# Kernel optimization log

Measured on AMD Instinct MI355X. Metric: run time of the kernel, lower is better.

## Reference

```python
import jax, jax.numpy as jnp
from jax import lax
import numpy as np

B, E, K, CAP = 512, 16, 2, 64
H = W = 32
ALPHA, LOAD_PEN, MIN_USE, RTEMP = 0.7, 2.0, 0.05, 1.0


def _conv(x, w, b):
    y = lax.conv_general_dilated(x, w, (1, 1), 'SAME', dimension_numbers=('NCHW', 'OIHW', 'NCHW'))
    return y + b[None, :, None, None]


def _bn(x, s, b):
    # eval-mode BatchNorm2d: running_mean=0, running_var=1 folded into scale/bias
    return x * s[None, :, None, None] + b[None, :, None, None]


def _ln(x, g, b, eps=1e-5):
    m = x.mean(-1, keepdims=True)
    v = ((x - m) ** 2).mean(-1, keepdims=True)
    return (x - m) * lax.rsqrt(v + eps) * g + b


def _maxpool(x):
    return lax.reduce_window(x, -jnp.inf, lax.max, (1, 1, 2, 2), (1, 1, 2, 2), 'VALID')


def setup_inputs() -> dict:
    key = jax.random.key(0)
    ks = iter(jax.random.split(key, 64))

    def nrm(shape, fan_in):
        return jax.random.normal(next(ks), shape, jnp.float32) / float(np.sqrt(fan_in))

    inp = {'x': jax.random.normal(next(ks), (B, 3, H, W), jnp.float32)}
    for i, (ci, co) in enumerate([(3, 64), (64, 64), (64, 128), (128, 128), (128, 256), (256, 256)], 1):
        inp[f'conv_w{i}'] = nrm((co, ci, 3, 3), ci * 9)
        inp[f'conv_b{i}'] = jnp.zeros((co,), jnp.float32)
        inp[f'bn_s{i}'] = jnp.ones((co,), jnp.float32)
        inp[f'bn_b{i}'] = jnp.zeros((co,), jnp.float32)
    inp['gate_w1'] = nrm((E, 64, 256), 256); inp['gate_b1'] = jnp.zeros((E, 64)); inp['gate_g1'] = jnp.ones((E, 64)); inp['gate_bb1'] = jnp.zeros((E, 64))
    inp['gate_w2'] = nrm((E, 32, 64), 64); inp['gate_b2'] = jnp.zeros((E, 32))
    inp['gate_w3'] = nrm((E, 1, 32), 32); inp['gate_b3'] = jnp.zeros((E, 1))
    inp['exp_w1'] = nrm((E, 256, 256), 256); inp['exp_b1'] = jnp.zeros((E, 256)); inp['exp_g1'] = jnp.ones((E, 256)); inp['exp_bb1'] = jnp.zeros((E, 256))
    inp['exp_w2'] = nrm((E, 128, 256), 256); inp['exp_b2'] = jnp.zeros((E, 128)); inp['exp_g2'] = jnp.ones((E, 128)); inp['exp_bb2'] = jnp.zeros((E, 128))
    inp['exp_w3'] = nrm((E, 128, 128), 128); inp['exp_b3'] = jnp.zeros((E, 128))
    inp['cls_w'] = nrm((E, 10, 128), 128); inp['cls_b'] = jnp.zeros((E, 10))
    return inp


def _forward(x, conv_w1, conv_b1, bn_s1, bn_b1, conv_w2, conv_b2, bn_s2, bn_b2,
             conv_w3, conv_b3, bn_s3, bn_b3, conv_w4, conv_b4, bn_s4, bn_b4,
             conv_w5, conv_b5, bn_s5, bn_b5, conv_w6, conv_b6, bn_s6, bn_b6,
             gate_w1, gate_b1, gate_g1, gate_bb1, gate_w2, gate_b2, gate_w3, gate_b3,
             exp_w1, exp_b1, exp_g1, exp_bb1, exp_w2, exp_b2, exp_g2, exp_bb2,
             exp_w3, exp_b3, cls_w, cls_b):
    # ---- trunk (eval: dropout = identity) ----
    h = jax.nn.relu(_bn(_conv(x, conv_w1, conv_b1), bn_s1, bn_b1))
    h = jax.nn.relu(_bn(_conv(h, conv_w2, conv_b2), bn_s2, bn_b2))
    h = _maxpool(h)
    h = jax.nn.relu(_bn(_conv(h, conv_w3, conv_b3), bn_s3, bn_b3))
    h = jax.nn.relu(_bn(_conv(h, conv_w4, conv_b4), bn_s4, bn_b4))
    h = _maxpool(h)
    h = jax.nn.relu(_bn(_conv(h, conv_w5, conv_b5), bn_s5, bn_b5))
    h = jax.nn.relu(_bn(_conv(h, conv_w6, conv_b6), bn_s6, bn_b6))
    feats = h.mean((2, 3))  # AdaptiveAvgPool2d(1) + Flatten -> [B, 256]
    # ---- experts (vectorized over E) ----
    h1 = jax.nn.relu(_ln(jnp.einsum('bc,eoc->beo', feats, exp_w1) + exp_b1, exp_g1, exp_bb1))
    h2 = jax.nn.relu(_ln(jnp.einsum('beh,eoh->beo', h1, exp_w2) + exp_b2, exp_g2, exp_bb2))
    embeds = jnp.einsum('beh,eoh->beo', h2, exp_w3) + exp_b3  # [B, E, 128]
    logits_e = jnp.einsum('bed,ecd->bec', embeds, cls_w) + cls_b  # [B, E, 10]
    probs = jax.nn.softmax(logits_e, axis=2)
    entropy = -(probs * jnp.log(probs + 1e-12)).sum(-1)  # [B, E]
    confidence = -entropy
    # ---- gates (vectorized over E) ----
    g1 = jax.nn.relu(_ln(jnp.einsum('bc,eoc->beo', feats, gate_w1) + gate_b1, gate_g1, gate_bb1))
    g2 = jax.nn.relu(jnp.einsum('beh,eoh->beo', g1, gate_w2) + gate_b2)
    scores = (jnp.einsum('beh,eoh->beo', g2, gate_w3) + gate_b3)[..., 0] / RTEMP  # [B, E]
    # ---- top-k capacity routing (eval: usage_ema at init = 1/E, no noise) ----
    usage = jnp.full((E,), 1.0 / E, jnp.float32)
    combined = ALPHA * scores + (1.0 - ALPHA) * confidence
    combined = combined + jnp.where(usage < MIN_USE, (MIN_USE - usage) * 10.0, 0.0)[None, :]
    balanced = combined - LOAD_PEN * usage[None, :]
    _, topk_idx = lax.top_k(balanced, K)  # [B, K]

    def step(loads, idx_row):
        lt = loads[idx_row]  # [K]
        avail = lt < CAP
        chosen = jnp.where(jnp.any(avail), idx_row[jnp.argmax(avail)], idx_row[jnp.argmin(lt)])
        return loads.at[chosen].add(1.0), chosen

    _, chosen = lax.scan(step, jnp.zeros((E,), jnp.float32), topk_idx)
    D = jax.nn.one_hot(chosen, E, dtype=jnp.bool_)  # [B, E]
    masked = jnp.where(D, balanced, -jnp.inf)
    rw = jax.nn.softmax(masked, axis=1) * D
    rw = rw / (rw.sum(1, keepdims=True) + 1e-12)
    final_logits = jnp.einsum('be,bec->bc', rw, logits_e)
    return final_logits, balanced, D


def reference(x, conv_w1, conv_b1, bn_s1, bn_b1, conv_w2, conv_b2, bn_s2, bn_b2,
              conv_w3, conv_b3, bn_s3, bn_b3, conv_w4, conv_b4, bn_s4, bn_b4,
              conv_w5, conv_b5, bn_s5, bn_b5, conv_w6, conv_b6, bn_s6, bn_b6,
              gate_w1, gate_b1, gate_g1, gate_bb1, gate_w2, gate_b2, gate_w3, gate_b3,
              exp_w1, exp_b1, exp_g1, exp_bb1, exp_w2, exp_b2, exp_g2, exp_bb2,
              exp_w3, exp_b3, cls_w, cls_b):
    return _forward(x, conv_w1, conv_b1, bn_s1, bn_b1, conv_w2, conv_b2, bn_s2, bn_b2,
                    conv_w3, conv_b3, bn_s3, bn_b3, conv_w4, conv_b4, bn_s4, bn_b4,
                    conv_w5, conv_b5, bn_s5, bn_b5, conv_w6, conv_b6, bn_s6, bn_b6,
                    gate_w1, gate_b1, gate_g1, gate_bb1, gate_w2, gate_b2, gate_w3, gate_b3,
                    exp_w1, exp_b1, exp_g1, exp_bb1, exp_w2, exp_b2, exp_g2, exp_bb2,
                    exp_w3, exp_b3, cls_w, cls_b)
```

## Files before the change

kernel.cpp:

```cpp
#include <hip/hip_runtime.h>


typedef _Float16 h16;
typedef _Float16 half8 __attribute__((ext_vector_type(8)));
typedef float f32x16 __attribute__((ext_vector_type(16)));

__device__ __forceinline__ void split2f(float x, h16& hh, h16& ll) {
  h16 a = (h16)x;
  hh = a;
  ll = (h16)(x - (float)a);
}

__global__ void prep_all_k(const float* __restrict__ cw1, const float* __restrict__ cw2,
                           const float* __restrict__ cw3, const float* __restrict__ cw4,
                           const float* __restrict__ cw5, const float* __restrict__ cw6,
                           float* __restrict__ wt1t, h16* __restrict__ wh,
                           h16* p0, h16* p1, h16* p2, h16* p3) {
  int idx = blockIdx.x * 256 + threadIdx.x;
  if (idx < 64) {
    h16* p = (idx < 16) ? p0 : (idx < 32) ? p1 : (idx < 48) ? p2 : p3;
    p[idx & 15] = (h16)0.f;
    return;
  }
  idx -= 64;
  if (idx < 1728) {
    int co = idx % 64, r = idx / 64;
    wt1t[idx] = cw1[(size_t)co * 27 + r];
    return;
  }
  idx -= 1728;
  const float* w; int CIN, COUT; size_t off;
  if (idx < 36864)        { w = cw2; CIN = 64;  COUT = 64;  off = 0; }
  else if (idx < 110592)  { w = cw3; CIN = 64;  COUT = 128; off = 36864;  idx -= 36864; }
  else if (idx < 258048)  { w = cw4; CIN = 128; COUT = 128; off = 110592; idx -= 110592; }
  else if (idx < 552960)  { w = cw5; CIN = 128; COUT = 256; off = 258048; idx -= 258048; }
  else if (idx < 1142784) { w = cw6; CIN = 256; COUT = 256; off = 552960; idx -= 552960; }
  else return;
  int KCOB = COUT >> 6;
  int lidx = idx;
  int c8   = idx & 7;
  int t    = idx >> 3;
  int co64 = t & 63;  t >>= 6;
  int half = t & 1;   t >>= 1;
  int cob  = t % KCOB; t /= KCOB;
  int tap  = t % 9;
  int ck   = t / 9;
  int ci = ck * 16 + half * 8 + c8;
  int co = cob * 64 + co64;
  float v = w[((size_t)co * CIN + ci) * 9 + tap];
  wh[off + lidx] = (h16)v;
}

__global__ __launch_bounds__(256) void conv1_k(
    const float* __restrict__ x, const float* __restrict__ wt,
    const float* __restrict__ cb, const float* __restrict__ bns,
    const float* __restrict__ bnb, h16* __restrict__ oh, h16* __restrict__ ol)
{
  __shared__ float sx[3 * 34 * 34];
  const int tid = threadIdx.x;
  const int img = blockIdx.x;
  for (int idx = tid; idx < 3 * 34 * 34; idx += 256) {
    int xx = idx % 34;
    int t  = idx / 34;
    int rr = t % 34;
    int c  = t / 34;
    int gr = rr - 1, gx = xx - 1;
    float v = 0.f;
    if (gr >= 0 && gr < 32 && gx >= 0 && gx < 32)
      v = x[((size_t)(img * 3 + c) * 32 + gr) * 32 + gx];
    sx[(c * 34 + rr) * 34 + xx] = v;
  }
  __syncthreads();
#pragma unroll 1
  for (int k = 0; k < 4; ++k) {
    int px = k * 256 + tid;
    int yy = px >> 5, xx = px & 31;
    float in27[27];
#pragma unroll
    for (int c = 0; c < 3; ++c)
#pragma unroll
      for (int dy = 0; dy < 3; ++dy)
#pragma unroll
        for (int dx = 0; dx < 3; ++dx)
          in27[c * 9 + dy * 3 + dx] = sx[(c * 34 + yy + dy) * 34 + xx + dx];
#pragma unroll 1
    for (int cbk = 0; cbk < 4; ++cbk) {
      h16 hb[16], lb[16];
#pragma unroll
      for (int j = 0; j < 16; ++j) {
        int co = cbk * 16 + j;
        float acc = 0.f;
#pragma unroll
        for (int t = 0; t < 27; ++t) acc = fmaf(in27[t], wt[t * 64 + co], acc);
        float s = bns[co];
        float yv = fmaxf(fmaf(acc + cb[co], s, bnb[co]), 0.f);
        split2f(yv, hb[j], lb[j]);
      }
      size_t o = 16 + ((size_t)(img * 4 + cbk) * 1024 + px) * 16;
      *(half8*)&oh[o]     = *(half8*)&hb[0];
      *(half8*)&oh[o + 8] = *(half8*)&hb[8];
      *(half8*)&ol[o]     = *(half8*)&lb[0];
      *(half8*)&ol[o + 8] = *(half8*)&lb[8];
    }
  }
}

template<int H, int W, int CIN, int COUT, int MT, int POOL, int OCC>
__global__ __launch_bounds__(256, OCC) void conv_mfma(
    const h16* __restrict__ Ah, const h16* __restrict__ Al,
    const h16* __restrict__ Wh,
    const float* __restrict__ cb, const float* __restrict__ bns,
    const float* __restrict__ bnb,
    h16* __restrict__ Oh, h16* __restrict__ Ol, float* __restrict__ feats)
{
  constexpr int TPI  = (H * W) / 32;
  constexpr int RPT  = 32 / W;
  constexpr int IPB  = (4 * MT * 32 >= H * W) ? (4 * MT * 32) / (H * W) : 1;
  constexpr int KC   = CIN / 16;
  constexpr int HW   = H * W;
  constexpr int KCO  = COUT / 16;
  constexpr int KCOB = COUT / 64;
  constexpr int LOGW = (W == 32) ? 5 : (W == 16) ? 4 : 3;
  constexpr int PF   = (MT == 1) ? 3 : 2;

  __shared__ h16 sBh[2][9 * 2 * 64 * 8];
  __shared__ float sRed[(POOL == 2 && MT == 1) ? 256 : 1];

  const int tid  = threadIdx.x;
  const int lane = tid & 63;
  const int wave = tid >> 6;
  const int half = lane >> 5;
  const int col  = lane & 31;
  const int cob  = blockIdx.z;
  const int co0  = cob * 64;

  int aoff[MT], ty[MT], tx[MT], img_t[MT], rw0[MT];
#pragma unroll
  for (int t = 0; t < MT; ++t) {
    int gt   = blockIdx.y * (4 * MT) + wave * MT + t;
    int img  = blockIdx.x * IPB + gt / TPI;
    int row0 = (gt % TPI) * RPT;
    int y = row0 + (col >> LOGW);
    int x = col & (W - 1);
    img_t[t] = img; rw0[t] = row0; ty[t] = y; tx[t] = x;
    aoff[t] = 16 + ((img * KC) * HW + y * W + x) * 16 + half * 8;
  }

  f32x16 acc[MT][2];
#pragma unroll
  for (int t = 0; t < MT; ++t)
#pragma unroll
    for (int n = 0; n < 2; ++n)
#pragma unroll
      for (int i = 0; i < 16; ++i) acc[t][n][i] = 0.f;

#pragma unroll
  for (int i = 0; i < 5; ++i) {
    int id = tid + i * 256;
    if (id < 1152) {
      int src = ((0 * 9 + (id >> 7)) * KCOB + cob) * 1024 + (id & 127) * 8;
      *(half8*)&sBh[0][id * 8] = *(const half8*)(Wh + src);
    }
  }
  __syncthreads();

  int buf = 0;
#pragma unroll 1
  for (int ck = 0; ck < KC; ++ck) {
    half8 stg[5];
    const bool have_next = (ck + 1 < KC);
    if (have_next) {
#pragma unroll
      for (int i = 0; i < 5; ++i) {
        int id = tid + i * 256;
        if (id < 1152) {
          int src = (((ck + 1) * 9 + (id >> 7)) * KCOB + cob) * 1024 + (id & 127) * 8;
          stg[i] = *(const half8*)(Wh + src);
        }
      }
    }

    const int ckoA = ck * (HW * 16);
    const h16* bB = sBh[buf];

    half8 pah[PF][MT], pal[PF][MT];
#pragma unroll
    for (int pt = 0; pt < PF; ++pt) {
      const int dy = pt / 3 - 1, dx = pt % 3 - 1;
      const int ashift = (dy * W + dx) * 16;
#pragma unroll
      for (int t = 0; t < MT; ++t) {
        bool v = ((unsigned)(ty[t] + dy) < (unsigned)H) &&
                 ((unsigned)(tx[t] + dx) < (unsigned)W);
        int ai = v ? (aoff[t] + ckoA + ashift) : (half * 8);
        pah[pt][t] = *(const half8*)(Ah + ai);
        pal[pt][t] = *(const half8*)(Al + ai);
      }
    }

#pragma unroll
    for (int tap = 0; tap < 9; ++tap) {
      const int bufr = tap % PF;
      half8 bh[2];
#pragma unroll
      for (int n = 0; n < 2; ++n) {
        int bi = ((tap * 2 + half) * 64 + n * 32 + col) * 8;
        bh[n] = *(const half8*)&bB[bi];
      }
      half8 cah[MT], cal[MT];
#pragma unroll
      for (int t = 0; t < MT; ++t) { cah[t] = pah[bufr][t]; cal[t] = pal[bufr][t]; }
      if (tap + PF < 9) {
        const int pt = tap + PF;
        const int dy = pt / 3 - 1, dx = pt % 3 - 1;
        const int ashift = (dy * W + dx) * 16;
#pragma unroll
        for (int t = 0; t < MT; ++t) {
          bool v = ((unsigned)(ty[t] + dy) < (unsigned)H) &&
                   ((unsigned)(tx[t] + dx) < (unsigned)W);
          int ai = v ? (aoff[t] + ckoA + ashift) : (half * 8);
          pah[bufr][t] = *(const half8*)(Ah + ai);
          pal[bufr][t] = *(const half8*)(Al + ai);
        }
      }
#pragma unroll
      for (int t = 0; t < MT; ++t)
#pragma unroll
        for (int n = 0; n < 2; ++n) {
          acc[t][n] = __builtin_amdgcn_mfma_f32_32x32x16_f16(cah[t], bh[n], acc[t][n], 0, 0, 0);
          acc[t][n] = __builtin_amdgcn_mfma_f32_32x32x16_f16(cal[t], bh[n], acc[t][n], 0, 0, 0);
        }
    }

    if (have_next) {
#pragma unroll
      for (int i = 0; i < 5; ++i) {
        int id = tid + i * 256;
        if (id < 1152)
          *(half8*)&sBh[buf ^ 1][id * 8] = stg[i];
      }
    }
    __syncthreads();
    buf ^= 1;
  }

#pragma unroll
  for (int n = 0; n < 2; ++n) {
    const int co = co0 + n * 32 + col;
    const float es = bns[co];
    const float eb = fmaf(cb[co], es, bnb[co]);
    const int cko = co >> 4, c16 = co & 15;

    if constexpr (POOL == 0) {
#pragma unroll
      for (int t = 0; t < MT; ++t) {
#pragma unroll
        for (int r = 0; r < 16; ++r) {
          float v = fmaxf(fmaf(acc[t][n][r], es, eb), 0.f);
          int m = (r & 3) + 4 * half + 8 * (r >> 2);
          int y = rw0[t] + (m >> LOGW);
          int x = m & (W - 1);
          size_t oi = 16 + ((size_t)(img_t[t] * KCO + cko) * HW + y * W + x) * 16 + c16;
          h16 hh, ll; split2f(v, hh, ll);
          Oh[oi] = hh; Ol[oi] = ll;
        }
      }
    } else if constexpr (POOL == 1 && RPT == 1) {
      constexpr int HWq = (H / 2) * (W / 2);
#pragma unroll
      for (int tp = 0; tp < MT / 2; ++tp) {
        const int t0 = 2 * tp, t1 = 2 * tp + 1;
        const int yq = rw0[t0] >> 1;
#pragma unroll
        for (int r = 0; r < 16; r += 2) {
          float v00 = fmaxf(fmaf(acc[t0][n][r],     es, eb), 0.f);
          float v01 = fmaxf(fmaf(acc[t0][n][r + 1], es, eb), 0.f);
          float v10 = fmaxf(fmaf(acc[t1][n][r],     es, eb), 0.f);
          float v11 = fmaxf(fmaf(acc[t1][n][r + 1], es, eb), 0.f);
          float mv = fmaxf(fmaxf(v00, v01), fmaxf(v10, v11));
          int xq = ((r & 3) >> 1) + 2 * half + 4 * (r >> 2);
          size_t oi = 16 + ((size_t)(img_t[t0] * KCO + cko) * HWq + yq * (W / 2) + xq) * 16 + c16;
          h16 hh, ll; split2f(mv, hh, ll);
          Oh[oi] = hh; Ol[oi] = ll;
        }
      }
    } else if constexpr (POOL == 1) {
      constexpr int HWq = (H / 2) * (W / 2);
#pragma unroll
      for (int t = 0; t < MT; ++t) {
        const int yq = rw0[t] >> 1;
#pragma unroll
        for (int r = 0; r < 8; r += 2) {
          float v00 = fmaxf(fmaf(acc[t][n][r],     es, eb), 0.f);
          float v01 = fmaxf(fmaf(acc[t][n][r + 1], es, eb), 0.f);
          float v10 = fmaxf(fmaf(acc[t][n][r + 8], es, eb), 0.f);
          float v11 = fmaxf(fmaf(acc[t][n][r + 9], es, eb), 0.f);
          float mv = fmaxf(fmaxf(v00, v01), fmaxf(v10, v11));
          int xq = ((r & 3) >> 1) + 2 * half + 4 * (r >> 2);
          size_t oi = 16 + ((size_t)(img_t[t] * KCO + cko) * HWq + yq * (W / 2) + xq) * 16 + c16;
          h16 hh, ll; split2f(mv, hh, ll);
          Oh[oi] = hh; Ol[oi] = ll;
        }
      }
    } else if constexpr (POOL == 2 && MT == 1) {
      float s = 0.f;
#pragma unroll
      for (int r = 0; r < 16; ++r)
        s += fmaxf(fmaf(acc[0][n][r], es, eb), 0.f);
      s += __shfl_xor(s, 32, 64);
      if (half == 0) sRed[wave * 64 + n * 32 + col] = s;
    } else if constexpr (POOL == 2) {
      float s = 0.f;
#pragma unroll
      for (int t = 0; t < MT; ++t)
#pragma unroll
        for (int r = 0; r < 16; ++r)
          s += fmaxf(fmaf(acc[t][n][r], es, eb), 0.f);
      s += __shfl_xor(s, 32, 64);
      if (half == 0) feats[(size_t)img_t[0] * 256 + co] = s * (1.f / 64.f);
    }
  }

  if constexpr (POOL == 2 && MT == 1) {
    __syncthreads();
    if (tid < 128) {
      int li = tid >> 6, co_l = tid & 63;
      float s = sRed[(li * 2) * 64 + co_l] + sRed[(li * 2 + 1) * 64 + co_l];
      feats[(size_t)(blockIdx.x * 2 + li) * 256 + co0 + co_l] = s * (1.f / 64.f);
    }
  }
}

template<int O, int K, int LN, int RELU>
__global__ __launch_bounds__(256, 4) void gemm_head(
    const float* __restrict__ A, size_t aStrideE,
    const float* __restrict__ Wm, const float* __restrict__ bias,
    const float* __restrict__ g, const float* __restrict__ bb,
    float* __restrict__ out)
{
  constexpr int KC  = (O >= 256) ? 32 : 64;
  constexpr int WST = O + 4;
  constexpr int TO  = O / 16;
  __shared__ float sA[KC * 36];
  __shared__ float sW[KC * WST];
  __shared__ float mArr[32], rArr[32];

  const int tid  = threadIdx.x;
  const int lane = tid & 63;
  const int wave = tid >> 6;
  const int e    = blockIdx.y;
  const int b0g  = blockIdx.x * 32;
  const int bl   = (lane & 15) * 2;
  const int ol   = wave * (O / 4) + (lane >> 4) * TO;

  const float* Ae = A + (size_t)e * aStrideE;
  const float* We = Wm + (size_t)e * O * K;

  float acc[2][TO];
#pragma unroll
  for (int i = 0; i < 2; ++i)
#pragma unroll
    for (int j = 0; j < TO; ++j) acc[i][j] = 0.f;

  for (int k0 = 0; k0 < K; k0 += KC) {
    for (int idx = tid; idx < 32 * KC; idx += 256) {
      int kk = idx % KC, bb_ = idx / KC;
      sA[kk * 36 + bb_] = Ae[(size_t)(b0g + bb_) * K + k0 + kk];
    }
    for (int idx = tid; idx < O * KC; idx += 256) {
      int kk = idx % KC, oo = idx / KC;
      sW[kk * WST + oo] = We[(size_t)oo * K + k0 + kk];
    }
    __syncthreads();
#pragma unroll 4
    for (int kk = 0; kk < KC; ++kk) {
      float2 av = *(const float2*)&sA[kk * 36 + bl];
      float a2[2] = {av.x, av.y};
#pragma unroll
      for (int j4 = 0; j4 < TO; j4 += 4) {
        float4 wv = *(const float4*)&sW[kk * WST + ol + j4];
        float w4[4] = {wv.x, wv.y, wv.z, wv.w};
#pragma unroll
        for (int i = 0; i < 2; ++i)
#pragma unroll
          for (int jj = 0; jj < 4; ++jj)
            acc[i][j4 + jj] = fmaf(a2[i], w4[jj], acc[i][j4 + jj]);
      }
    }
    __syncthreads();
  }

  const float* bi = bias + (size_t)e * O;
#pragma unroll
  for (int i = 0; i < 2; ++i)
#pragma unroll
    for (int j = 0; j < TO; ++j) acc[i][j] += bi[ol + j];

  if constexpr (LN) {
    float* redS = sA;
    float* redQ = sA + 512;
    const int grp = wave * 4 + (lane >> 4);
#pragma unroll
    for (int i = 0; i < 2; ++i) {
      float s = 0.f, q = 0.f;
#pragma unroll
      for (int j = 0; j < TO; ++j) { s += acc[i][j]; q += acc[i][j] * acc[i][j]; }
      redS[(bl + i) * 16 + grp] = s;
      redQ[(bl + i) * 16 + grp] = q;
    }
    __syncthreads();
    if (tid < 32) {
      float s = 0.f, q = 0.f;
#pragma unroll
      for (int gi = 0; gi < 16; ++gi) { s += redS[tid * 16 + gi]; q += redQ[tid * 16 + gi]; }
      float mean = s * (1.f / O);
      float var  = q * (1.f / O) - mean * mean;
      mArr[tid] = mean;
      rArr[tid] = rsqrtf(var + 1e-5f);
    }
    __syncthreads();
    const float* gp  = g + (size_t)e * O;
    const float* bbp = bb + (size_t)e * O;
#pragma unroll
    for (int i = 0; i < 2; ++i) {
      float mean = mArr[bl + i], rstd = rArr[bl + i];
#pragma unroll
      for (int j = 0; j < TO; ++j)
        acc[i][j] = (acc[i][j] - mean) * rstd * gp[ol + j] + bbp[ol + j];
    }
  }
  if constexpr (RELU) {
#pragma unroll
    for (int i = 0; i < 2; ++i)
#pragma unroll
      for (int j = 0; j < TO; ++j) acc[i][j] = fmaxf(acc[i][j], 0.f);
  }
#pragma unroll
  for (int i = 0; i < 2; ++i) {
    float* op = out + ((size_t)e * 512 + b0g + bl + i) * O + ol;
#pragma unroll
    for (int j4 = 0; j4 < TO; j4 += 4)
      *(float4*)(op + j4) = make_float4(acc[i][j4], acc[i][j4 + 1], acc[i][j4 + 2], acc[i][j4 + 3]);
  }
}

__global__ void cls_softmax_k(const float* __restrict__ embeds,
                              const float* __restrict__ cw,
                              const float* __restrict__ cbias,
                              float* __restrict__ logits_e,
                              float* __restrict__ conf)
{
  int wv   = (blockIdx.x * 256 + threadIdx.x) >> 6;
  int lane = threadIdx.x & 63;
  int b = wv >> 4, e = wv & 15;
  const float* ep = embeds + ((size_t)e * 512 + b) * 128;
  float e0 = ep[lane], e1 = ep[lane + 64];
  float l[10];
#pragma unroll
  for (int o = 0; o < 10; ++o) {
    const float* wp = cw + ((size_t)e * 10 + o) * 128;
    l[o] = e0 * wp[lane] + e1 * wp[lane + 64];
  }
#pragma unroll
  for (int s = 32; s >= 1; s >>= 1)
#pragma unroll
    for (int o = 0; o < 10; ++o) l[o] += __shfl_xor(l[o], s, 64);
#pragma unroll
  for (int o = 0; o < 10; ++o) l[o] += cbias[e * 10 + o];
  float m = l[0];
#pragma unroll
  for (int o = 1; o < 10; ++o) m = fmaxf(m, l[o]);
  float p[10], sum = 0.f;
#pragma unroll
  for (int o = 0; o < 10; ++o) { p[o] = expf(l[o] - m); sum += p[o]; }
  float inv = 1.f / sum, ent = 0.f;
#pragma unroll
  for (int o = 0; o < 10; ++o) { float pp = p[o] * inv; ent -= pp * logf(pp + 1e-12f); }
  if (lane == 0) {
    conf[b * 16 + e] = -ent;
#pragma unroll
    for (int o = 0; o < 10; ++o) logits_e[((size_t)b * 16 + e) * 10 + o] = l[o];
  }
}

__global__ void gate23_k(const float* __restrict__ g1, const float* __restrict__ w2,
                         const float* __restrict__ b2, const float* __restrict__ w3,
                         const float* __restrict__ b3, float* __restrict__ scores)
{
  int wv   = (blockIdx.x * 256 + threadIdx.x) >> 6;
  int lane = threadIdx.x & 63;
  int b = wv >> 4, e = wv & 15;
  float gv = g1[((size_t)e * 512 + b) * 64 + lane];
  const float* w3p = w3 + e * 32;
  float sc = 0.f;
#pragma unroll
  for (int o = 0; o < 32; ++o) {
    float t = gv * w2[((size_t)e * 32 + o) * 64 + lane];
#pragma unroll
    for (int s = 32; s >= 1; s >>= 1) t += __shfl_xor(t, s, 64);
    float g2v = fmaxf(t + b2[e * 32 + o], 0.f);
    sc = fmaf(g2v, w3p[o], sc);
  }
  if (lane == 0) scores[b * 16 + e] = sc + b3[e];
}

__global__ void routing_k(const float* __restrict__ scores, const float* __restrict__ conf,
                          const float* __restrict__ logits_e, float* __restrict__ out)
{
  __shared__ int t2[512];
  __shared__ int chs[512];
  const int tid = threadIdx.x;

  if (tid < 512) {
    int b = tid;
    float v0 = -3.4e38f, v1 = -3.4e38f;
    int i0 = 0, i1 = 0;
#pragma unroll
    for (int e = 0; e < 16; ++e) {
      float s = scores[b * 16 + e];
      float c = conf[b * 16 + e];
      float v = 0.7f * s + 0.3f * c - 0.125f;
      out[5120 + b * 16 + e] = v;
      if (v > v0) { v1 = v0; i1 = i0; v0 = v; i0 = e; }
      else if (v > v1) { v1 = v; i1 = e; }
    }
    t2[b] = i0 | (i1 << 8);
  }
  __syncthreads();

  if (tid < 64) {
    int lane = tid;
    int cnt = 0;
    int pk[8];
#pragma unroll
    for (int k = 0; k < 8; ++k) pk[k] = t2[k * 64 + lane];
#pragma unroll 1
    for (int k = 0; k < 8; ++k) {
      for (int j = 0; j < 64; ++j) {
        int pair = __shfl(pk[k], j, 64);
        int i0 = pair & 0xff, i1 = (pair >> 8) & 0xff;
        int c0 = __shfl(cnt, i0, 64);
        int c1 = __shfl(cnt, i1, 64);
        int ch = (c0 < 64) ? i0 : ((c1 < 64) ? i1 : ((c0 <= c1) ? i0 : i1));
        cnt += (lane == ch) ? 1 : 0;
        if (lane == 0) chs[k * 64 + j] = ch;
      }
    }
  }
  __syncthreads();

  if (tid < 512) {
    int b = tid;
    int ch = chs[b];
#pragma unroll
    for (int e = 0; e < 16; ++e)
      out[13312 + b * 16 + e] = (e == ch) ? 1.0f : 0.0f;
#pragma unroll
    for (int o = 0; o < 10; ++o)
      out[b * 10 + o] = logits_e[((size_t)b * 16 + ch) * 10 + o];
  }
}

extern "C" void kernel_launch(void* const* d_in, const int* in_sizes, int n_in,
                              void* d_out, int out_size, void* d_ws, size_t ws_size,
                              hipStream_t stream) {
  (void)in_sizes; (void)n_in; (void)out_size; (void)ws_size;

  const float* x = (const float*)d_in[0];
  const float *cw[6], *cbv[6], *bsv[6], *bbv[6];
  for (int i = 0; i < 6; ++i) {
    cw[i]  = (const float*)d_in[1 + 4 * i];
    cbv[i] = (const float*)d_in[2 + 4 * i];
    bsv[i] = (const float*)d_in[3 + 4 * i];
    bbv[i] = (const float*)d_in[4 + 4 * i];
  }
  const float* gate_w1  = (const float*)d_in[25];
  const float* gate_b1  = (const float*)d_in[26];
  const float* gate_g1  = (const float*)d_in[27];
  const float* gate_bb1 = (const float*)d_in[28];
  const float* gate_w2  = (const float*)d_in[29];
  const float* gate_b2  = (const float*)d_in[30];
  const float* gate_w3  = (const float*)d_in[31];
  const float* gate_b3  = (const float*)d_in[32];
  const float* exp_w1   = (const float*)d_in[33];
  const float* exp_b1   = (const float*)d_in[34];
  const float* exp_g1   = (const float*)d_in[35];
  const float* exp_bb1  = (const float*)d_in[36];
  const float* exp_w2   = (const float*)d_in[37];
  const float* exp_b2   = (const float*)d_in[38];
  const float* exp_g2   = (const float*)d_in[39];
  const float* exp_bb2  = (const float*)d_in[40];
  const float* exp_w3   = (const float*)d_in[41];
  const float* exp_b3   = (const float*)d_in[42];
  const float* cls_w    = (const float*)d_in[43];
  const float* cls_b    = (const float*)d_in[44];

  char* wsb = (char*)d_ws;
  const size_t off_wt1t = 0;
  const size_t off_whi  = 6912;
  const size_t off_Phi  = 4578048;
  const size_t off_Plo  = 71687168;
  const size_t off_Qhi  = 138796288;
  const size_t off_Qlo  = 155573760;
  const size_t off_feats= 172351232;
  const size_t off_h1   = 138796288 + 512;
  const size_t off_h2   = off_h1 + 8388608;
  const size_t off_emb  = off_h2 + 4194304;
  const size_t off_g1   = off_emb + 4194304;
  const size_t off_lg   = off_g1 + 2097152;
  const size_t off_conf = off_lg + 327680;
  const size_t off_sc   = off_conf + 32768;

  float* wt1t = (float*)(wsb + off_wt1t);
  h16* whi = (h16*)(wsb + off_whi);
  h16* Phi = (h16*)(wsb + off_Phi);
  h16* Plo = (h16*)(wsb + off_Plo);
  h16* Qhi = (h16*)(wsb + off_Qhi);
  h16* Qlo = (h16*)(wsb + off_Qlo);
  float* feats = (float*)(wsb + off_feats);
  float* h1 = (float*)(wsb + off_h1);
  float* h2 = (float*)(wsb + off_h2);
  float* emb = (float*)(wsb + off_emb);
  float* g1 = (float*)(wsb + off_g1);
  float* lg = (float*)(wsb + off_lg);
  float* conf = (float*)(wsb + off_conf);
  float* sc = (float*)(wsb + off_sc);

  const size_t wo2 = 0;
  const size_t wo3 = 36864;
  const size_t wo4 = 110592;
  const size_t wo5 = 258048;
  const size_t wo6 = 552960;

  prep_all_k<<<4471, 256, 0, stream>>>(cw[0], cw[1], cw[2], cw[3], cw[4], cw[5],
                                       wt1t, whi, Phi, Plo, Qhi, Qlo);

  conv1_k<<<512, 256, 0, stream>>>(x, wt1t, cbv[0], bsv[0], bbv[0], Phi, Plo);
  conv_mfma<32, 32, 64, 64, 2, 1, 3><<<dim3(512, 4, 1), 256, 0, stream>>>(
      Phi, Plo, whi + wo2, cbv[1], bsv[1], bbv[1], Qhi, Qlo, nullptr);
  conv_mfma<16, 16, 64, 128, 2, 0, 3><<<dim3(512, 1, 2), 256, 0, stream>>>(
      Qhi, Qlo, whi + wo3, cbv[2], bsv[2], bbv[2], Phi, Plo, nullptr);
  conv_mfma<16, 16, 128, 128, 2, 1, 3><<<dim3(512, 1, 2), 256, 0, stream>>>(
      Phi, Plo, whi + wo4, cbv[3], bsv[3], bbv[3], Qhi, Qlo, nullptr);
  conv_mfma<8, 8, 128, 256, 1, 0, 4><<<dim3(256, 1, 4), 256, 0, stream>>>(
      Qhi, Qlo, whi + wo5, cbv[4], bsv[4], bbv[4], Phi, Plo, nullptr);
  conv_mfma<8, 8, 256, 256, 1, 2, 4><<<dim3(256, 1, 4), 256, 0, stream>>>(
      Phi, Plo, whi + wo6, cbv[5], bsv[5], bbv[5], nullptr, nullptr, feats);

  gemm_head<256, 256, 1, 1><<<dim3(16, 16), 256, 0, stream>>>(
      feats, (size_t)0, exp_w1, exp_b1, exp_g1, exp_bb1, h1);
  gemm_head<128, 256, 1, 1><<<dim3(16, 16), 256, 0, stream>>>(
      h1, (size_t)512 * 256, exp_w2, exp_b2, exp_g2, exp_bb2, h2);
  gemm_head<128, 128, 0, 0><<<dim3(16, 16), 256, 0, stream>>>(
      h2, (size_t)512 * 128, exp_w3, exp_b3, nullptr, nullptr, emb);
  cls_softmax_k<<<2048, 256, 0, stream>>>(emb, cls_w, cls_b, lg, conf);

  gemm_head<64, 256, 1, 1><<<dim3(16, 16), 256, 0, stream>>>(
      feats, (size_t)0, gate_w1, gate_b1, gate_g1, gate_bb1, g1);
  gate23_k<<<2048, 256, 0, stream>>>(g1, gate_w2, gate_b2, gate_w3, gate_b3, sc);

  routing_k<<<1, 512, 0, stream>>>(sc, conf, lg, (float*)d_out);
}
```

Baseline: 728.9 us.

## Stream conv weights directly into LDS and merge small head kernels

The conv MFMA kernel now loads each next weight slab straight from global memory into the alternate LDS buffer with global_load_lds. This replaces staging the slab in registers and writing it out after the compute loop, which cuts register pressure and VGPR-to-LDS store instructions. The classifier-softmax and gate layer-2/3 kernels are also fused into one launch, and the gate layer-1 GEMM is moved earlier, removing one kernel launch. A risk is that the async LDS writes have no explicit vmcnt wait before the barrier, so correctness depends on the compiler inserting proper waits.

```diff
diff --git a/kernel.cpp b/kernel.cpp
--- a/kernel.cpp
+++ b/kernel.cpp
@@ -9,6 +9,12 @@
   h16 a = (h16)x;
   hh = a;
   ll = (h16)(x - (float)a);
+}
+
+__device__ __forceinline__ void dma_b16(const h16* g, h16* l) {
+  __builtin_amdgcn_global_load_lds(
+      (const __attribute__((address_space(1))) void*)g,
+      (__attribute__((address_space(3))) void*)l, 16, 0, 0);
 }
 
 __global__ void prep_all_k(const float* __restrict__ cw1, const float* __restrict__ cw2,
@@ -158,8 +164,8 @@
   for (int i = 0; i < 5; ++i) {
     int id = tid + i * 256;
     if (id < 1152) {
-      int src = ((0 * 9 + (id >> 7)) * KCOB + cob) * 1024 + (id & 127) * 8;
-      *(half8*)&sBh[0][id * 8] = *(const half8*)(Wh + src);
+      int src = ((id >> 7) * KCOB + cob) * 1024 + (id & 127) * 8;
+      dma_b16(Wh + src, &sBh[0][id * 8]);
     }
   }
   __syncthreads();
@@ -167,7 +173,6 @@
   int buf = 0;
 #pragma unroll 1
   for (int ck = 0; ck < KC; ++ck) {
-    half8 stg[5];
     const bool have_next = (ck + 1 < KC);
     if (have_next) {
 #pragma unroll
@@ -175,7 +180,7 @@
         int id = tid + i * 256;
         if (id < 1152) {
           int src = (((ck + 1) * 9 + (id >> 7)) * KCOB + cob) * 1024 + (id & 127) * 8;
-          stg[i] = *(const half8*)(Wh + src);
+          dma_b16(Wh + src, &sBh[buf ^ 1][id * 8]);
         }
       }
     }
@@ -232,14 +237,6 @@
         }
     }
 
-    if (have_next) {
-#pragma unroll
-      for (int i = 0; i < 5; ++i) {
-        int id = tid + i * 256;
-        if (id < 1152)
-          *(half8*)&sBh[buf ^ 1][id * 8] = stg[i];
-      }
-    }
     __syncthreads();
     buf ^= 1;
   }
@@ -444,15 +441,19 @@
   }
 }
 
-__global__ void cls_softmax_k(const float* __restrict__ embeds,
+__global__ void heads_small_k(const float* __restrict__ embeds,
                               const float* __restrict__ cw,
                               const float* __restrict__ cbias,
-                              float* __restrict__ logits_e,
-                              float* __restrict__ conf)
+                              const float* __restrict__ g1, const float* __restrict__ w2,
+                              const float* __restrict__ b2, const float* __restrict__ w3,
+                              const float* __restrict__ b3,
+                              float* __restrict__ logits_e, float* __restrict__ conf,
+                              float* __restrict__ scores)
 {
   int wv   = (blockIdx.x * 256 + threadIdx.x) >> 6;
   int lane = threadIdx.x & 63;
   int b = wv >> 4, e = wv & 15;
+
   const float* ep = embeds + ((size_t)e * 512 + b) * 128;
   float e0 = ep[lane], e1 = ep[lane + 64];
   float l[10];
@@ -481,15 +482,7 @@
 #pragma unroll
     for (int o = 0; o < 10; ++o) logits_e[((size_t)b * 16 + e) * 10 + o] = l[o];
   }
-}
-
-__global__ void gate23_k(const float* __restrict__ g1, const float* __restrict__ w2,
-                         const float* __restrict__ b2, const float* __restrict__ w3,
-                         const float* __restrict__ b3, float* __restrict__ scores)
-{
-  int wv   = (blockIdx.x * 256 + threadIdx.x) >> 6;
-  int lane = threadIdx.x & 63;
-  int b = wv >> 4, e = wv & 15;
+
   float gv = g1[((size_t)e * 512 + b) * 64 + lane];
   const float* w3p = w3 + e * 32;
   float sc = 0.f;
@@ -649,15 +642,15 @@
 
   gemm_head<256, 256, 1, 1><<<dim3(16, 16), 256, 0, stream>>>(
       feats, (size_t)0, exp_w1, exp_b1, exp_g1, exp_bb1, h1);
+  gemm_head<64, 256, 1, 1><<<dim3(16, 16), 256, 0, stream>>>(
+      feats, (size_t)0, gate_w1, gate_b1, gate_g1, gate_bb1, g1);
   gemm_head<128, 256, 1, 1><<<dim3(16, 16), 256, 0, stream>>>(
       h1, (size_t)512 * 256, exp_w2, exp_b2, exp_g2, exp_bb2, h2);
   gemm_head<128, 128, 0, 0><<<dim3(16, 16), 256, 0, stream>>>(
       h2, (size_t)512 * 128, exp_w3, exp_b3, nullptr, nullptr, emb);
-  cls_softmax_k<<<2048, 256, 0, stream>>>(emb, cls_w, cls_b, lg, conf);
-
-  gemm_head<64, 256, 1, 1><<<dim3(16, 16), 256, 0, stream>>>(
-      feats, (size_t)0, gate_w1, gate_b1, gate_g1, gate_bb1, g1);
-  gate23_k<<<2048, 256, 0, stream>>>(g1, gate_w2, gate_b2, gate_w3, gate_b3, sc);
+  heads_small_k<<<2048, 256, 0, stream>>>(emb, cls_w, cls_b,
+                                          g1, gate_w2, gate_b2, gate_w3, gate_b3,
+                                          lg, conf, sc);
 
   routing_k<<<1, 512, 0, stream>>>(sc, conf, lg, (float*)d_out);
 }
```

New measurement: 725.7 us. About the same (-0.4%).
